# Kernel tuning notes

Hardware: AMD Instinct MI355X
Metric: run time of the kernel (lower is better)

The kernel has to match this reference:

```python
import jax, jax.numpy as jnp
import numpy as np

N_NODES = 100000
N_EDGES = 1_600_000
IN_DIM, HID, OUT_DIM, N_BLOCKS = 963, 192, 3, 6


def spmm(src, dst, w, x):
    # sparse adj @ x, adj[dst, src] = w  (COO edge list)
    msgs = x[src] * w[:, None]                      # [E, F]
    return jax.ops.segment_sum(msgs, dst, num_segments=N_NODES)


def gconv(x, src, dst, ew, w, lw, b):
    # Pixel2Mesh GConv: adj @ (x @ W) + x @ W_loop + b
    return spmm(src, dst, ew, x @ w) + x @ lw + b


def setup_inputs() -> dict:
    key = jax.random.key(0)
    ks = jax.random.split(key, 13)
    s = 0.02  # small init scale to keep deep stack numerically tame
    return {
        "inputs": jax.random.normal(ks[0], (N_NODES, IN_DIM), jnp.float32),
        "edge_src": jax.random.randint(ks[1], (N_EDGES,), 0, N_NODES),
        "edge_dst": jax.random.randint(ks[2], (N_EDGES,), 0, N_NODES),
        "edge_weight": jax.random.uniform(ks[3], (N_EDGES,), jnp.float32) / 16.0,
        "w_in": jax.random.normal(ks[4], (IN_DIM, HID), jnp.float32) * s,
        "loop_in": jax.random.normal(ks[5], (IN_DIM, HID), jnp.float32) * s,
        "b_in": jnp.zeros((HID,), jnp.float32),
        "blocks_w": jax.random.normal(ks[6], (N_BLOCKS, 2, HID, HID), jnp.float32) * s,
        "blocks_loop": jax.random.normal(ks[7], (N_BLOCKS, 2, HID, HID), jnp.float32) * s,
        "blocks_b": jnp.zeros((N_BLOCKS, 2, HID), jnp.float32),
        "w_out": jax.random.normal(ks[8], (HID, OUT_DIM), jnp.float32) * s,
        "loop_out": jax.random.normal(ks[9], (HID, OUT_DIM), jnp.float32) * s,
        "b_out": jnp.zeros((OUT_DIM,), jnp.float32),
    }


def reference(inputs, edge_src, edge_dst, edge_weight, w_in, loop_in, b_in,
              blocks_w, blocks_loop, blocks_b, w_out, loop_out, b_out):
    x = gconv(inputs, edge_src, edge_dst, edge_weight, w_in, loop_in, b_in)

    def block(x, params):
        bw, bl, bb = params
        h = gconv(x, edge_src, edge_dst, edge_weight, bw[0], bl[0], bb[0])
        h = gconv(h, edge_src, edge_dst, edge_weight, bw[1], bl[1], bb[1])
        return (x + h) * 0.5, None

    x_cat, _ = jax.lax.scan(block, x, (blocks_w, blocks_loop, blocks_b))
    x_out = gconv(x_cat, edge_src, edge_dst, edge_weight, w_out, loop_out, b_out)
    return (x_out, x_cat)
```

## Files before the change

kernel.cpp:

```cpp
#include <hip/hip_runtime.h>
#include <cstdint>
#include <cstddef>

#define N_NODES 100000
#define N_EDGES 1600000
#define IN_DIM 963
#define HID 192
#define OUT_DIM 3

typedef _Float16 f16x8 __attribute__((ext_vector_type(8)));
typedef float f32x4 __attribute__((ext_vector_type(4)));

__global__ void count_kernel(const int* __restrict__ dst, int* __restrict__ counts, int E) {
    int i = blockIdx.x * blockDim.x + threadIdx.x;
    if (i < E) atomicAdd(&counts[dst[i]], 1);
}

__global__ void scan_kernel(const int* __restrict__ counts, int* __restrict__ row_ptr, int n) {
    __shared__ int buf[1024];
    __shared__ int carry_s;
    int t = threadIdx.x;
    if (t == 0) { carry_s = 0; row_ptr[0] = 0; }
    __syncthreads();
    for (int base = 0; base < n; base += 1024) {
        int idx = base + t;
        int v = (idx < n) ? counts[idx] : 0;
        buf[t] = v;
        __syncthreads();
        for (int off = 1; off < 1024; off <<= 1) {
            int add = (t >= off) ? buf[t - off] : 0;
            __syncthreads();
            buf[t] += add;
            __syncthreads();
        }
        int carry = carry_s;
        if (idx < n) row_ptr[idx + 1] = carry + buf[t];
        __syncthreads();
        if (t == 1023) carry_s = carry + buf[1023];
        __syncthreads();
    }
}

__global__ void copy_cursor_kernel(const int* __restrict__ rp, int* __restrict__ cursor, int n) {
    int i = blockIdx.x * blockDim.x + threadIdx.x;
    if (i < n) cursor[i] = rp[i];
}

__global__ void scatter_kernel(const int* __restrict__ src, const int* __restrict__ dst,
                               const float* __restrict__ w, int* __restrict__ cursor,
                               int* __restrict__ csr_src, float* __restrict__ csr_w,
                               int* __restrict__ csr_eid, int E) {
    int i = blockIdx.x * blockDim.x + threadIdx.x;
    if (i < E) {
        int d = dst[i];
        int p = atomicAdd(&cursor[d], 1);
        csr_src[p] = src[i];
        csr_w[p] = w[i];
        csr_eid[p] = i;
    }
}

__global__ void sortrow_kernel(const int* __restrict__ rp, int* __restrict__ csr_src,
                               float* __restrict__ csr_w, int* __restrict__ csr_eid, int n) {
    int r = blockIdx.x * blockDim.x + threadIdx.x;
    if (r >= n) return;
    int s = rp[r], e = rp[r + 1];
    for (int i = s + 1; i < e; ++i) {
        int ke = csr_eid[i]; int ks = csr_src[i]; float kw = csr_w[i];
        int j = i - 1;
        while (j >= s && csr_eid[j] > ke) {
            csr_eid[j + 1] = csr_eid[j];
            csr_src[j + 1] = csr_src[j];
            csr_w[j + 1] = csr_w[j];
            --j;
        }
        csr_eid[j + 1] = ke; csr_src[j + 1] = ks; csr_w[j + 1] = kw;
    }
}

__global__ __launch_bounds__(256)
void trans_split(const float* __restrict__ W, const float* __restrict__ L,
                 int K, int Kp, _Float16* __restrict__ out_hi, _Float16* __restrict__ out_lo) {
    __shared__ float tile[32][33];
    const int n0 = blockIdx.x * 32, k0 = blockIdx.y * 32;
    const int tx = threadIdx.x, ty = threadIdx.y;
#pragma unroll
    for (int i = 0; i < 4; ++i) {
        int k = k0 + ty + i * 8;
        int n = n0 + tx;
        float v = 0.f;
        if (k < K) v = (n < HID) ? W[(size_t)k * HID + n] : L[(size_t)k * HID + (n - HID)];
        tile[ty + i * 8][tx] = v;
    }
    __syncthreads();
#pragma unroll
    for (int i = 0; i < 4; ++i) {
        int nl = ty + i * 8;
        int n = n0 + nl;
        int k = k0 + tx;
        float v = tile[tx][nl];
        _Float16 hi = (_Float16)v;
        _Float16 lo = (_Float16)(v - (float)hi);
        out_hi[(size_t)n * Kp + k] = hi;
        out_lo[(size_t)n * Kp + k] = lo;
    }
}

__global__ __launch_bounds__(256, 2)
void gemm_lds(const float* __restrict__ X, int M, int Kx, int Kp,
              const _Float16* __restrict__ Wth, const _Float16* __restrict__ Wtl,
              const float* __restrict__ bias, const float* __restrict__ res,
              float* __restrict__ Hdst, float* __restrict__ Tdst) {
    __shared__ __align__(16) char smem[81920];

    const int m0 = blockIdx.x * 128;
    const int tid = threadIdx.x;
    const int lane = tid & 63;
    const int wave = tid >> 6;
    const int wr = wave >> 1;
    const int wc = wave & 1;
    const int kg = lane >> 4;
    const int bcol = blockIdx.y * 192;

    auto stage = [&](int k0, int cb) {
#pragma unroll
        for (int i = 0; i < 4; ++i) {
            const int id = i * 256 + tid;
            const int row = id >> 3, slot = id & 7;
            int gr = m0 + row; if (gr >= M) gr = 0;
            const int srck = k0 + ((slot ^ (row & 7)) << 2);
            const float* src = X + (size_t)gr * Kx + srck;
            void* dst = (void*)(smem + cb + (i * 256 + wave * 64) * 16);
            __builtin_amdgcn_global_load_lds(
                (const __attribute__((address_space(1))) void*)src,
                (__attribute__((address_space(3))) void*)dst, 16, 0, 0);
        }
#pragma unroll
        for (int i = 0; i < 3; ++i) {
            const int id = i * 256 + tid;
            const int row = id >> 2, slot = id & 3;
            const int srck = k0 + ((slot ^ ((row >> 1) & 3)) << 3);
            const size_t go = (size_t)(bcol + row) * Kp + srck;
            void* dsth = (void*)(smem + cb + 16384 + (i * 256 + wave * 64) * 16);
            void* dstl = (void*)(smem + cb + 28672 + (i * 256 + wave * 64) * 16);
            __builtin_amdgcn_global_load_lds(
                (const __attribute__((address_space(1))) void*)(Wth + go),
                (__attribute__((address_space(3))) void*)dsth, 16, 0, 0);
            __builtin_amdgcn_global_load_lds(
                (const __attribute__((address_space(1))) void*)(Wtl + go),
                (__attribute__((address_space(3))) void*)dstl, 16, 0, 0);
        }
    };

    f32x4 acc[4][6];
#pragma unroll
    for (int i = 0; i < 4; ++i)
#pragma unroll
        for (int j = 0; j < 6; ++j)
            acc[i][j] = f32x4{0.f, 0.f, 0.f, 0.f};

    const int nsteps = (Kx + 31) / 32;

    stage(0, 0);
    __syncthreads();

    for (int s = 0; s < nsteps; ++s) {
        const int cb = (s & 1) * 40960;
        if (s + 1 < nsteps) stage((s + 1) * 32, ((s + 1) & 1) * 40960);

        const char* cur = smem + cb;
        f16x8 fah[4], fal[4];
#pragma unroll
        for (int mi = 0; mi < 4; ++mi) {
            const int row = wr * 64 + mi * 16 + (lane & 15);
            const char* rb = cur + row * 128;
            f32x4 a0 = *(const f32x4*)(rb + ((((2 * kg)     ^ (row & 7))) << 4));
            f32x4 a1 = *(const f32x4*)(rb + ((((2 * kg + 1) ^ (row & 7))) << 4));
            f16x8 hi, lo;
#pragma unroll
            for (int j = 0; j < 4; ++j) {
                float x0 = a0[j], x1 = a1[j];
                _Float16 h0 = (_Float16)x0, h1 = (_Float16)x1;
                hi[j] = h0;     hi[4 + j] = h1;
                lo[j] = (_Float16)(x0 - (float)h0);
                lo[4 + j] = (_Float16)(x1 - (float)h1);
            }
            fah[mi] = hi; fal[mi] = lo;
        }
#pragma unroll
        for (int ni = 0; ni < 6; ++ni) {
            const int idx = wc * 96 + ni * 16 + (lane & 15);
            const int off = 16384 + idx * 64 + ((kg ^ ((idx >> 1) & 3)) << 4);
            const f16x8 fbh = *(const f16x8*)(cur + off);
            const f16x8 fbl = *(const f16x8*)(cur + off + 12288);
#pragma unroll
            for (int mi = 0; mi < 4; ++mi)
                acc[mi][ni] = __builtin_amdgcn_mfma_f32_16x16x32_f16(fah[mi], fbh, acc[mi][ni], 0, 0, 0);
#pragma unroll
            for (int mi = 0; mi < 4; ++mi)
                acc[mi][ni] = __builtin_amdgcn_mfma_f32_16x16x32_f16(fal[mi], fbh, acc[mi][ni], 0, 0, 0);
#pragma unroll
            for (int mi = 0; mi < 4; ++mi)
                acc[mi][ni] = __builtin_amdgcn_mfma_f32_16x16x32_f16(fah[mi], fbl, acc[mi][ni], 0, 0, 0);
        }
        __syncthreads();
    }

    const bool isH = (bcol == 0);
#pragma unroll
    for (int mi = 0; mi < 4; ++mi) {
        const int rbase = m0 + wr * 64 + mi * 16 + ((lane >> 4) << 2);
#pragma unroll
        for (int ni = 0; ni < 6; ++ni) {
            const int gc = wc * 96 + ni * 16 + (lane & 15);
            f32x4 v = acc[mi][ni];
            if (isH) {
#pragma unroll
                for (int j = 0; j < 4; ++j) {
                    const int row = rbase + j;
                    if (row < M) Hdst[(size_t)row * HID + gc] = v[j];
                }
            } else {
                const float bv = bias[gc];
#pragma unroll
                for (int j = 0; j < 4; ++j) {
                    const int row = rbase + j;
                    if (row < M) {
                        float t = v[j] + bv;
                        if (res != nullptr) t += res[(size_t)row * HID + gc];
                        Tdst[(size_t)row * HID + gc] = t;
                    }
                }
            }
        }
    }
}

__global__ __launch_bounds__(256, 8)
void spmm_kernel(const int* __restrict__ rp, const int* __restrict__ csrc,
                 const float* __restrict__ cw, const float* __restrict__ Hm,
                 float* __restrict__ out, float scale) {
    const int lane = threadIdx.x & 63;
    const int nwaves = (gridDim.x * blockDim.x) >> 6;
    for (int wid = (blockIdx.x * blockDim.x + threadIdx.x) >> 6; wid < N_NODES;
         wid += nwaves) {
        const int s = __builtin_amdgcn_readfirstlane(rp[wid]);
        const int e = __builtin_amdgcn_readfirstlane(rp[wid + 1]);
        float a0 = 0.f, a1 = 0.f, a2 = 0.f;
        int i = s;
        for (; i + 7 < e; i += 8) {
            float w[8];
            const float* h[8];
#pragma unroll
            for (int u = 0; u < 8; ++u) {
                w[u] = cw[i + u];
                h[u] = Hm + (size_t)csrc[i + u] * HID;
            }
#pragma unroll
            for (int u = 0; u < 8; ++u) {
                float x0 = h[u][lane], x1 = h[u][64 + lane], x2 = h[u][128 + lane];
                a0 += w[u] * x0; a1 += w[u] * x1; a2 += w[u] * x2;
            }
        }
        for (; i + 3 < e; i += 4) {
            float w[4];
            const float* h[4];
#pragma unroll
            for (int u = 0; u < 4; ++u) {
                w[u] = cw[i + u];
                h[u] = Hm + (size_t)csrc[i + u] * HID;
            }
#pragma unroll
            for (int u = 0; u < 4; ++u) {
                float x0 = h[u][lane], x1 = h[u][64 + lane], x2 = h[u][128 + lane];
                a0 += w[u] * x0; a1 += w[u] * x1; a2 += w[u] * x2;
            }
        }
        for (; i < e; ++i) {
            float w = cw[i];
            const float* h = Hm + (size_t)csrc[i] * HID;
            a0 += w * h[lane];
            a1 += w * h[64 + lane];
            a2 += w * h[128 + lane];
        }
        float* o = out + (size_t)wid * HID;
        o[lane]       = scale * (o[lane] + a0);
        o[64 + lane]  = scale * (o[64 + lane] + a1);
        o[128 + lane] = scale * (o[128 + lane] + a2);
    }
}

__global__ __launch_bounds__(256)
void out_gemm(const float* __restrict__ X, const float* __restrict__ Wout,
              const float* __restrict__ Lout, const float* __restrict__ bout,
              float* __restrict__ H3, float* __restrict__ T3) {
    __shared__ float Ws[HID * OUT_DIM];
    __shared__ float Ls[HID * OUT_DIM];
    int tid = threadIdx.x;
    for (int i = tid; i < HID * OUT_DIM; i += 256) { Ws[i] = Wout[i]; Ls[i] = Lout[i]; }
    __syncthreads();
    int n = blockIdx.x * 4 + (tid >> 6);
    int lane = tid & 63;
    if (n >= N_NODES) return;
    const float* x = X + (size_t)n * HID;
    float aw[3] = {0.f, 0.f, 0.f}, al[3] = {0.f, 0.f, 0.f};
#pragma unroll
    for (int p = 0; p < 3; ++p) {
        int k = p * 64 + lane;
        float xv = x[k];
#pragma unroll
        for (int c = 0; c < 3; ++c) {
            aw[c] += xv * Ws[k * 3 + c];
            al[c] += xv * Ls[k * 3 + c];
        }
    }
#pragma unroll
    for (int off = 32; off > 0; off >>= 1) {
#pragma unroll
        for (int c = 0; c < 3; ++c) {
            aw[c] += __shfl_down(aw[c], off, 64);
            al[c] += __shfl_down(al[c], off, 64);
        }
    }
    if (lane == 0) {
#pragma unroll
        for (int c = 0; c < 3; ++c) {
            H3[n * 3 + c] = aw[c];
            T3[n * 3 + c] = al[c] + bout[c];
        }
    }
}

__global__ __launch_bounds__(256)
void out_spmm(const int* __restrict__ rp, const int* __restrict__ csrc,
              const float* __restrict__ cw, const float* __restrict__ H3,
              const float* __restrict__ T3, float* __restrict__ out) {
    int n = blockIdx.x * blockDim.x + threadIdx.x;
    if (n >= N_NODES) return;
    int s = rp[n], e = rp[n + 1];
    float a0 = 0.f, a1 = 0.f, a2 = 0.f;
    for (int i = s; i < e; ++i) {
        float w = cw[i];
        int src = csrc[i];
        a0 += w * H3[src * 3 + 0];
        a1 += w * H3[src * 3 + 1];
        a2 += w * H3[src * 3 + 2];
    }
    out[n * 3 + 0] = a0 + T3[n * 3 + 0];
    out[n * 3 + 1] = a1 + T3[n * 3 + 1];
    out[n * 3 + 2] = a2 + T3[n * 3 + 2];
}

extern "C" void kernel_launch(void* const* d_in, const int* in_sizes, int n_in,
                              void* d_out, int out_size, void* d_ws, size_t ws_size,
                              hipStream_t stream) {
    const float* X0    = (const float*)d_in[0];
    const int*   esrc  = (const int*)d_in[1];
    const int*   edst  = (const int*)d_in[2];
    const float* ew    = (const float*)d_in[3];
    const float* w_in  = (const float*)d_in[4];
    const float* l_in  = (const float*)d_in[5];
    const float* b_in  = (const float*)d_in[6];
    const float* bw    = (const float*)d_in[7];
    const float* bl    = (const float*)d_in[8];
    const float* bb    = (const float*)d_in[9];
    const float* w_out = (const float*)d_in[10];
    const float* l_out = (const float*)d_in[11];
    const float* b_out = (const float*)d_in[12];

    char* ws = (char*)d_ws;
    size_t off = 0;
    auto alloc = [&](size_t bytes) -> void* {
        void* p = ws + off;
        off += (bytes + 255) & ~(size_t)255;
        return p;
    };
    float* Hbuf   = (float*)alloc(sizeof(float) * (size_t)N_NODES * HID);
    float* h1     = (float*)alloc(sizeof(float) * (size_t)N_NODES * HID);
    int*   counts = (int*)alloc(sizeof(int) * N_NODES);
    int*   rp     = (int*)alloc(sizeof(int) * (N_NODES + 1));
    int*   cursor = (int*)alloc(sizeof(int) * N_NODES);
    int*   csrc   = (int*)alloc(sizeof(int) * N_EDGES);
    float* cw     = (float*)alloc(sizeof(float) * N_EDGES);
    int*   ceid   = (int*)alloc(sizeof(int) * N_EDGES);
    float* H3     = (float*)alloc(sizeof(float) * (size_t)N_NODES * OUT_DIM);
    float* T3     = (float*)alloc(sizeof(float) * (size_t)N_NODES * OUT_DIM);
    const int KP0 = 992;
    _Float16* Wt0h = (_Float16*)alloc(sizeof(_Float16) * 384 * KP0);
    _Float16* Wt0l = (_Float16*)alloc(sizeof(_Float16) * 384 * KP0);
    _Float16* WtHh = (_Float16*)alloc(sizeof(_Float16) * 12 * 384 * HID);
    _Float16* WtHl = (_Float16*)alloc(sizeof(_Float16) * 12 * 384 * HID);

    float* xout = (float*)d_out;
    float* xcat = (float*)d_out + (size_t)N_NODES * OUT_DIM;

    trans_split<<<dim3(12, 31), dim3(32, 8), 0, stream>>>(w_in, l_in, IN_DIM, KP0, Wt0h, Wt0l);
    for (int l = 0; l < 12; ++l) {
        trans_split<<<dim3(12, 6), dim3(32, 8), 0, stream>>>(
            bw + (size_t)l * HID * HID, bl + (size_t)l * HID * HID, HID, HID,
            WtHh + (size_t)l * 384 * HID, WtHl + (size_t)l * 384 * HID);
    }

    hipMemsetAsync(counts, 0, sizeof(int) * N_NODES, stream);
    count_kernel<<<(N_EDGES + 255) / 256, 256, 0, stream>>>(edst, counts, N_EDGES);
    scan_kernel<<<1, 1024, 0, stream>>>(counts, rp, N_NODES);
    copy_cursor_kernel<<<(N_NODES + 255) / 256, 256, 0, stream>>>(rp, cursor, N_NODES);
    scatter_kernel<<<(N_EDGES + 255) / 256, 256, 0, stream>>>(esrc, edst, ew, cursor,
                                                              csrc, cw, ceid, N_EDGES);
    sortrow_kernel<<<(N_NODES + 255) / 256, 256, 0, stream>>>(rp, csrc, cw, ceid, N_NODES);

    const dim3 gemm_grid((N_NODES + 127) / 128, 2);
    const int spmm_blocks = 2048;

    gemm_lds<<<gemm_grid, 256, 0, stream>>>(X0, N_NODES, IN_DIM, KP0, Wt0h, Wt0l,
                                            b_in, nullptr, Hbuf, xcat);
    spmm_kernel<<<spmm_blocks, 256, 0, stream>>>(rp, csrc, cw, Hbuf, xcat, 1.0f);

    for (int b = 0; b < 6; ++b) {
        int l0 = b * 2, l1 = b * 2 + 1;
        const float* B0 = bb + (size_t)l0 * HID;
        const float* B1 = bb + (size_t)l1 * HID;

        gemm_lds<<<gemm_grid, 256, 0, stream>>>(xcat, N_NODES, HID, HID,
                                                WtHh + (size_t)l0 * 384 * HID,
                                                WtHl + (size_t)l0 * 384 * HID,
                                                B0, nullptr, Hbuf, h1);
        spmm_kernel<<<spmm_blocks, 256, 0, stream>>>(rp, csrc, cw, Hbuf, h1, 1.0f);
        gemm_lds<<<gemm_grid, 256, 0, stream>>>(h1, N_NODES, HID, HID,
                                                WtHh + (size_t)l1 * 384 * HID,
                                                WtHl + (size_t)l1 * 384 * HID,
                                                B1, xcat, Hbuf, xcat);
        spmm_kernel<<<spmm_blocks, 256, 0, stream>>>(rp, csrc, cw, Hbuf, xcat, 0.5f);
    }

    out_gemm<<<(N_NODES + 3) / 4, 256, 0, stream>>>(xcat, w_out, l_out, b_out, H3, T3);
    out_spmm<<<(N_NODES + 255) / 256, 256, 0, stream>>>(rp, csrc, cw, H3, T3, xout);
}
```

Measured before the change: 4.739 ms.

## Parallelize row-pointer scan and split SpMM rows into per-channel wave tasks

Replaces the single-block serial prefix scan over node counts with a three-kernel multi-block scan (local block scans, a scan of block sums, then add-back). Splits each SpMM row into three 64-feature tasks handled by separate waves, with a 16-edge unrolled gather loop. This raises parallelism and memory-level parallelism in the gather. In exchange, the edge indices and weights of each row are now read three times, and a few more launches are added.

Result: faster. 4.548 ms (-4.0%).

```diff
diff --git a/kernel.cpp b/kernel.cpp
--- a/kernel.cpp
+++ b/kernel.cpp
@@ -16,29 +16,54 @@
     if (i < E) atomicAdd(&counts[dst[i]], 1);
 }
 
-__global__ void scan_kernel(const int* __restrict__ counts, int* __restrict__ row_ptr, int n) {
-    __shared__ int buf[1024];
-    __shared__ int carry_s;
-    int t = threadIdx.x;
-    if (t == 0) { carry_s = 0; row_ptr[0] = 0; }
+__global__ __launch_bounds__(256)
+void scan_local(const int* __restrict__ counts, int* __restrict__ rp,
+                int* __restrict__ bsum, int n) {
+    __shared__ int sm[256];
+    const int base = blockIdx.x * 1024;
+    const int t = threadIdx.x;
+    const int i0 = base + t * 4;
+    int v[4];
+#pragma unroll
+    for (int j = 0; j < 4; ++j) v[j] = (i0 + j < n) ? counts[i0 + j] : 0;
+    v[1] += v[0]; v[2] += v[1]; v[3] += v[2];
+    sm[t] = v[3];
     __syncthreads();
-    for (int base = 0; base < n; base += 1024) {
-        int idx = base + t;
-        int v = (idx < n) ? counts[idx] : 0;
-        buf[t] = v;
+    for (int off = 1; off < 256; off <<= 1) {
+        int add = (t >= off) ? sm[t - off] : 0;
         __syncthreads();
-        for (int off = 1; off < 1024; off <<= 1) {
-            int add = (t >= off) ? buf[t - off] : 0;
-            __syncthreads();
-            buf[t] += add;
-            __syncthreads();
-        }
-        int carry = carry_s;
-        if (idx < n) row_ptr[idx + 1] = carry + buf[t];
+        sm[t] += add;
         __syncthreads();
-        if (t == 1023) carry_s = carry + buf[1023];
+    }
+    const int pre = (t > 0) ? sm[t - 1] : 0;
+#pragma unroll
+    for (int j = 0; j < 4; ++j) {
+        int idx = i0 + j;
+        if (idx < n) rp[idx + 1] = pre + v[j];
+    }
+    if (t == 255) bsum[blockIdx.x] = sm[255];
+}
+
+__global__ __launch_bounds__(128)
+void scan_block(int* __restrict__ bsum, int nb) {
+    __shared__ int sm[128];
+    const int t = threadIdx.x;
+    const int v = (t < nb) ? bsum[t] : 0;
+    sm[t] = v;
+    __syncthreads();
+    for (int off = 1; off < 128; off <<= 1) {
+        int add = (t >= off) ? sm[t - off] : 0;
         __syncthreads();
-    }
+        sm[t] += add;
+        __syncthreads();
+    }
+    if (t < nb) bsum[t] = sm[t] - v;
+}
+
+__global__ void scan_add(const int* __restrict__ bsum, int* __restrict__ rp, int n) {
+    int i = blockIdx.x * blockDim.x + threadIdx.x;
+    if (i < n) rp[i + 1] += bsum[i >> 10];
+    if (i == 0) rp[0] = 0;
 }
 
 __global__ void copy_cursor_kernel(const int* __restrict__ rp, int* __restrict__ cursor, int n) {
@@ -242,51 +267,40 @@
                  float* __restrict__ out, float scale) {
     const int lane = threadIdx.x & 63;
     const int nwaves = (gridDim.x * blockDim.x) >> 6;
-    for (int wid = (blockIdx.x * blockDim.x + threadIdx.x) >> 6; wid < N_NODES;
-         wid += nwaves) {
+    const int ntasks = N_NODES * 3;
+    for (int task = (blockIdx.x * blockDim.x + threadIdx.x) >> 6; task < ntasks;
+         task += nwaves) {
+        const int wid = task / 3;
+        const int ch = task - wid * 3;
         const int s = __builtin_amdgcn_readfirstlane(rp[wid]);
         const int e = __builtin_amdgcn_readfirstlane(rp[wid + 1]);
-        float a0 = 0.f, a1 = 0.f, a2 = 0.f;
+        const int fo = ch * 64 + lane;
+        float a = 0.f;
         int i = s;
-        for (; i + 7 < e; i += 8) {
-            float w[8];
-            const float* h[8];
-#pragma unroll
-            for (int u = 0; u < 8; ++u) {
+        for (; i + 15 < e; i += 16) {
+            float w[16], x[16];
+#pragma unroll
+            for (int u = 0; u < 16; ++u) {
                 w[u] = cw[i + u];
-                h[u] = Hm + (size_t)csrc[i + u] * HID;
+                x[u] = Hm[(size_t)csrc[i + u] * HID + fo];
             }
 #pragma unroll
-            for (int u = 0; u < 8; ++u) {
-                float x0 = h[u][lane], x1 = h[u][64 + lane], x2 = h[u][128 + lane];
-                a0 += w[u] * x0; a1 += w[u] * x1; a2 += w[u] * x2;
-            }
+            for (int u = 0; u < 16; ++u) a += w[u] * x[u];
         }
         for (; i + 3 < e; i += 4) {
-            float w[4];
-            const float* h[4];
+            float w[4], x[4];
 #pragma unroll
             for (int u = 0; u < 4; ++u) {
                 w[u] = cw[i + u];
-                h[u] = Hm + (size_t)csrc[i + u] * HID;
+                x[u] = Hm[(size_t)csrc[i + u] * HID + fo];
             }
 #pragma unroll
-            for (int u = 0; u < 4; ++u) {
-                float x0 = h[u][lane], x1 = h[u][64 + lane], x2 = h[u][128 + lane];
-                a0 += w[u] * x0; a1 += w[u] * x1; a2 += w[u] * x2;
-            }
-        }
-        for (; i < e; ++i) {
-            float w = cw[i];
-            const float* h = Hm + (size_t)csrc[i] * HID;
-            a0 += w * h[lane];
-            a1 += w * h[64 + lane];
-            a2 += w * h[128 + lane];
-        }
-        float* o = out + (size_t)wid * HID;
-        o[lane]       = scale * (o[lane] + a0);
-        o[64 + lane]  = scale * (o[64 + lane] + a1);
-        o[128 + lane] = scale * (o[128 + lane] + a2);
+            for (int u = 0; u < 4; ++u) a += w[u] * x[u];
+        }
+        for (; i < e; ++i)
+            a += cw[i] * Hm[(size_t)csrc[i] * HID + fo];
+        float* o = out + (size_t)wid * HID + ch * 64;
+        o[lane] = scale * (o[lane] + a);
     }
 }
 
@@ -380,6 +394,7 @@
     int*   counts = (int*)alloc(sizeof(int) * N_NODES);
     int*   rp     = (int*)alloc(sizeof(int) * (N_NODES + 1));
     int*   cursor = (int*)alloc(sizeof(int) * N_NODES);
+    int*   bsum   = (int*)alloc(sizeof(int) * 128);
     int*   csrc   = (int*)alloc(sizeof(int) * N_EDGES);
     float* cw     = (float*)alloc(sizeof(float) * N_EDGES);
     int*   ceid   = (int*)alloc(sizeof(int) * N_EDGES);
@@ -401,9 +416,12 @@
             WtHh + (size_t)l * 384 * HID, WtHl + (size_t)l * 384 * HID);
     }
 
+    const int NB = (N_NODES + 1023) / 1024;
     hipMemsetAsync(counts, 0, sizeof(int) * N_NODES, stream);
     count_kernel<<<(N_EDGES + 255) / 256, 256, 0, stream>>>(edst, counts, N_EDGES);
-    scan_kernel<<<1, 1024, 0, stream>>>(counts, rp, N_NODES);
+    scan_local<<<NB, 256, 0, stream>>>(counts, rp, bsum, N_NODES);
+    scan_block<<<1, 128, 0, stream>>>(bsum, NB);
+    scan_add<<<(N_NODES + 255) / 256, 256, 0, stream>>>(bsum, rp, N_NODES);
     copy_cursor_kernel<<<(N_NODES + 255) / 256, 256, 0, stream>>>(rp, cursor, N_NODES);
     scatter_kernel<<<(N_EDGES + 255) / 256, 256, 0, stream>>>(esrc, edst, ew, cursor,
                                                               csrc, cw, ceid, N_EDGES);
```
